# Kernel optimization log

Measured on AMD Instinct MI355X. Metric: run time of the kernel, lower is better.

## Reference

```python
import jax, jax.numpy as jnp
import numpy as np

B = 16       # graphs per batch
N = 256      # nodes per graph (Hi-C submatrix bins)
NT = B * N   # total nodes
E = 131072   # total edges
DIN = 32     # input feature dim (HYPERPARAMETERS['input_shape'])
H1, H2 = 16, 32
HID = 32     # ContactCNN hidden dim
W7 = 7       # final conv width


def setup_inputs() -> dict:
    key = jax.random.key(0)
    ks = jax.random.split(key, 16)
    x = jax.random.normal(ks[0], (NT, DIN), dtype=jnp.float32)
    edge_index = jax.random.randint(ks[1], (2, E), 0, NT, dtype=jnp.int64)
    edge_attr = jax.random.uniform(ks[2], (E,), dtype=jnp.float32)
    batch_index = jnp.repeat(jnp.arange(B, dtype=jnp.int64), N)
    s = 0.1
    params = dict(
        W0=jax.random.normal(ks[3], (DIN, H1), dtype=jnp.float32) * s,
        b0=jnp.zeros((H1,), dtype=jnp.float32),
        W1=jax.random.normal(ks[4], (H1, H2), dtype=jnp.float32) * s,
        b1=jnp.zeros((H2,), dtype=jnp.float32),
        W2=jax.random.normal(ks[5], (H2, H2), dtype=jnp.float32) * s,
        b2=jnp.zeros((H2,), dtype=jnp.float32),
        Wc=jax.random.normal(ks[6], (HID, H2), dtype=jnp.float32) * s,  # 1x1 conv: [out=HID, in=H2]
        bc=jnp.zeros((HID,), dtype=jnp.float32),
        Wp=jax.random.normal(ks[7], (1, HID, W7, W7), dtype=jnp.float32) * s,  # OIHW
        bp=jnp.zeros((1,), dtype=jnp.float32),
    )
    return dict(x=x, edge_index=edge_index, edge_attr=edge_attr,
                batch_index=batch_index, **params)


def _gcn_norm(edge_index, edge_weight, n):
    # PyG gcn_norm with improved=True (self-loop fill value 2.0)
    src, dst = edge_index[0], edge_index[1]
    loop = jnp.arange(n, dtype=src.dtype)
    src_a = jnp.concatenate([src, loop])
    dst_a = jnp.concatenate([dst, loop])
    w_a = jnp.concatenate([edge_weight, jnp.full((n,), 2.0, dtype=edge_weight.dtype)])
    deg = jax.ops.segment_sum(w_a, dst_a, num_segments=n)
    deg_safe = jnp.where(deg > 0, deg, 1.0)
    dinv = jnp.where(deg > 0, jax.lax.rsqrt(deg_safe), 0.0)
    norm = dinv[src_a] * w_a * dinv[dst_a]
    return src_a, dst_a, norm


def _gcn_layer(h, W, b, src_a, dst_a, norm, n):
    h = h @ W                                  # [n, out]
    msg = norm[:, None] * h[src_a]             # gather + scale
    return jax.ops.segment_sum(msg, dst_a, num_segments=n) + b  # scatter-add


def reference(x, edge_index, edge_attr, batch_index,
              W0, b0, W1, b1, W2, b2, Wc, bc, Wp, bp):
    n = x.shape[0]
    src_a, dst_a, norm = _gcn_norm(edge_index, edge_attr, n)
    h = jax.nn.relu(_gcn_layer(x, W0, b0, src_a, dst_a, norm, n))
    h = jax.nn.relu(_gcn_layer(h, W1, b1, src_a, dst_a, norm, n))
    h = jax.nn.relu(_gcn_layer(h, W2, b2, src_a, dst_a, norm, n))
    z = h.reshape(B, N, -1)                    # process_graph_batch
    # ContactCNN: broadcast outer product -> 1x1 conv -> ReLU -> 7x7 conv -> sigmoid
    zm = jnp.einsum('bid,bjd->bdij', z, z)     # [B, D, N, N]
    c = jax.nn.relu(jnp.einsum('bdij,hd->bhij', zm, Wc) + bc[None, :, None, None])
    s = jax.lax.conv_general_dilated(
        c, Wp, window_strides=(1, 1), padding='SAME',
        dimension_numbers=('NCHW', 'OIHW', 'NCHW')) + bp[None, :, None, None]
    return jax.nn.sigmoid(s)                   # [B, 1, N, N]
```

## Files before the change

### kernel.cpp

```cpp
#include <hip/hip_runtime.h>
#include <hip/hip_bf16.h>
#include <hip/hip_fp16.h>

#define NT 4096
#define NE 131072

#define OFF_DEG    0
#define OFF_CNT    16384
#define OFF_FILL   32768
#define OFF_ROWPTR 49152
#define OFF_COL    66048
#define OFF_VAL    590336
#define OFF_G      1114624
#define OFF_HA     1638912
#define OFF_HB     2163200
#define OFF_W2     2687488
#define OFF_C      2695680

typedef __attribute__((ext_vector_type(8))) short bf16x8;
typedef __attribute__((ext_vector_type(4))) float f32x4;
typedef __attribute__((ext_vector_type(2))) __fp16 fp16x2;

__device__ inline unsigned int align16(unsigned int hi, unsigned int lo) {
#if __has_builtin(__builtin_amdgcn_alignbit)
    return __builtin_amdgcn_alignbit(hi, lo, 16);
#else
    return (lo >> 16) | (hi << 16);
#endif
}

__device__ inline unsigned short bfb(float x) {
    return __hip_bfloat16_raw(__float2bfloat16(x)).x;
}


__global__ void k_deg(const int* __restrict__ ei, const float* __restrict__ ew,
                      float* __restrict__ deg, int* __restrict__ cnt) {
    int e = blockIdx.x * 256 + threadIdx.x;
    if (e < NE) {
        int d = ei[NE + e];
        atomicAdd(&deg[d], ew[e]);
        atomicAdd(&cnt[d], 1);
    }
}

__global__ void k_scan(const int* __restrict__ cnt, int* __restrict__ rowptr,
                       float* __restrict__ deg, const float* __restrict__ Wp,
                       unsigned int* __restrict__ w2) {
    __shared__ int sums[1024];
    int t = threadIdx.x;
    #pragma unroll
    for (int k = 0; k < 4; k++) {
        int n = t*4 + k;
        deg[n] = rsqrtf(deg[n] + 2.0f);
    }
    for (int k = t; k < 1568; k += 1024) {
        __half h = __float2half(Wp[k]);
        __half2 hh = __halves2half2(h, h);
        w2[k] = *(unsigned int*)&hh;
    }
    int v0 = cnt[t*4], v1 = cnt[t*4+1], v2 = cnt[t*4+2], v3 = cnt[t*4+3];
    int s = v0 + v1 + v2 + v3;
    sums[t] = s;
    __syncthreads();
    for (int off = 1; off < 1024; off <<= 1) {
        int x = (t >= off) ? sums[t - off] : 0;
        __syncthreads();
        sums[t] += x;
        __syncthreads();
    }
    int excl = sums[t] - s;
    rowptr[t*4]   = excl;
    rowptr[t*4+1] = excl + v0;
    rowptr[t*4+2] = excl + v0 + v1;
    rowptr[t*4+3] = excl + v0 + v1 + v2;
    if (t == 1023) rowptr[NT] = excl + s;
}

__global__ void k_fill(const int* __restrict__ ei, const float* __restrict__ ew,
                       const float* __restrict__ dinv, const int* __restrict__ rowptr,
                       int* __restrict__ fill, int* __restrict__ col, float* __restrict__ val) {
    int e = blockIdx.x * 256 + threadIdx.x;
    if (e < NE) {
        int s = ei[e], d = ei[NE + e];
        int pos = rowptr[d] + atomicAdd(&fill[d], 1);
        col[pos] = s;
        val[pos] = dinv[s] * ew[e] * dinv[d];
    }
}


__global__ void k_mm0(const float* __restrict__ x, const float* __restrict__ W0,
                      float* __restrict__ g) {
    int tid = blockIdx.x * 256 + threadIdx.x;
    int n = tid >> 4, co = tid & 15;
    float acc = 0.f;
    #pragma unroll
    for (int ci = 0; ci < 32; ci++) acc += x[n*32 + ci] * W0[ci*16 + co];
    g[n*16 + co] = acc;
}

__global__ __launch_bounds__(256) void k_agg0(const float* __restrict__ g,
        const float* __restrict__ bias, const float* __restrict__ W1,
        const float* __restrict__ dinv, const int* __restrict__ rowptr,
        const int* __restrict__ col, const float* __restrict__ val,
        float* __restrict__ g1) {
    __shared__ float hs[8][2][16];
    int tid = threadIdx.x;
    int nl = tid >> 5, s = tid & 31, co = s & 15, half = s >> 4;
    int n = blockIdx.x*8 + nl;
    int e0 = rowptr[n], e1 = rowptr[n+1];
    float acc = 0.f;
    if (half == 0) { float dv = dinv[n]; acc = 2.f*dv*dv*g[n*16+co]; }
    int e = e0 + half;
    for (; e + 2 < e1; e += 4) {
        int   c0 = col[e], c1 = col[e+2];
        float v0 = val[e], v1 = val[e+2];
        acc += v0 * g[c0*16+co];
        acc += v1 * g[c1*16+co];
    }
    for (; e < e1; e += 2) acc += val[e] * g[col[e]*16+co];
    hs[nl][half][co] = acc;
    __syncthreads();
    int n2 = tid >> 5, c2 = tid & 31;
    float o = 0.f;
    #pragma unroll
    for (int ci = 0; ci < 16; ci++) {
        float h = fmaxf(hs[n2][0][ci] + hs[n2][1][ci] + bias[ci], 0.f);
        o += h * W1[ci*32 + c2];
    }
    g1[(blockIdx.x*8 + n2)*32 + c2] = o;
}

__global__ __launch_bounds__(256) void k_agg1(const float* __restrict__ g,
        const float* __restrict__ bias, const float* __restrict__ Wn,
        const float* __restrict__ dinv, const int* __restrict__ rowptr,
        const int* __restrict__ col, const float* __restrict__ val,
        float* __restrict__ gn) {
    __shared__ float hs[8][32];
    int tid = threadIdx.x;
    int nl = tid >> 5, co = tid & 31;
    int n = blockIdx.x*8 + nl;
    int e0 = rowptr[n], e1 = rowptr[n+1];
    float dv = dinv[n];
    float acc = 2.f*dv*dv*g[n*32+co];
    int e = e0;
    for (; e + 3 < e1; e += 4) {
        int   c0 = col[e], c1 = col[e+1], c2_ = col[e+2], c3 = col[e+3];
        float v0 = val[e], v1 = val[e+1], v2 = val[e+2], v3 = val[e+3];
        acc += v0 * g[c0*32+co];
        acc += v1 * g[c1*32+co];
        acc += v2 * g[c2_*32+co];
        acc += v3 * g[c3*32+co];
    }
    for (; e < e1; e++) acc += val[e] * g[col[e]*32+co];
    hs[nl][co] = acc;
    __syncthreads();
    float o = 0.f;
    #pragma unroll
    for (int ci = 0; ci < 32; ci++) {
        float h = fmaxf(hs[nl][ci] + bias[ci], 0.f);
        o += h * Wn[ci*32 + co];
    }
    gn[n*32 + co] = o;
}

__global__ __launch_bounds__(256) void k_agg2(const float* __restrict__ g,
        const float* __restrict__ bias,
        const float* __restrict__ dinv, const int* __restrict__ rowptr,
        const int* __restrict__ col, const float* __restrict__ val,
        float* __restrict__ h3) {
    int tid = blockIdx.x*256 + threadIdx.x;
    int n = tid >> 5, co = tid & 31;
    int e0 = rowptr[n], e1 = rowptr[n+1];
    float dv = dinv[n];
    float acc = 2.f*dv*dv*g[n*32+co];
    int e = e0;
    for (; e + 3 < e1; e += 4) {
        int   c0 = col[e], c1 = col[e+1], c2_ = col[e+2], c3 = col[e+3];
        float v0 = val[e], v1 = val[e+1], v2 = val[e+2], v3 = val[e+3];
        acc += v0 * g[c0*32+co];
        acc += v1 * g[c1*32+co];
        acc += v2 * g[c2_*32+co];
        acc += v3 * g[c3*32+co];
    }
    for (; e < e1; e++) acc += val[e] * g[col[e]*32+co];
    h3[n*32 + co] = fmaxf(acc + bias[co], 0.f);
}


__global__ __launch_bounds__(256) void k_c1(const float* __restrict__ z,
                                            const float* __restrict__ Wc,
                                            const float* __restrict__ bc,
                                            unsigned short* __restrict__ c) {
    __shared__ unsigned short zb[256*40];
    __shared__ unsigned short zwb[256*40];
    int blk = blockIdx.x;
    int b = blk >> 5, h = blk & 31;
    int tid = threadIdx.x;
    int lane = tid & 63, w = tid >> 6;
    int m = lane & 15, q = lane >> 4;

    {
        const float4* zp = (const float4*)&z[(b*256 + tid)*32];
        const float4* wp = (const float4*)&Wc[h*32];
        unsigned int ub[16], uw[16];
        #pragma unroll
        for (int r8 = 0; r8 < 8; r8++) {
            float4 f = zp[r8];
            float4 wv = wp[r8];
            ub[r8*2]   = ((unsigned int)bfb(f.y) << 16) | bfb(f.x);
            ub[r8*2+1] = ((unsigned int)bfb(f.w) << 16) | bfb(f.z);
            uw[r8*2]   = ((unsigned int)bfb(f.y*wv.y) << 16) | bfb(f.x*wv.x);
            uw[r8*2+1] = ((unsigned int)bfb(f.w*wv.w) << 16) | bfb(f.z*wv.z);
        }
        uint4* zbp = (uint4*)&zb[tid*40];
        uint4* zwp = (uint4*)&zwb[tid*40];
        #pragma unroll
        for (int k = 0; k < 4; k++) {
            zbp[k] = ((uint4*)ub)[k];
            zwp[k] = ((uint4*)uw)[k];
        }
    }
    __syncthreads();

    bf16x8 bt[16];
    #pragma unroll
    for (int nt = 0; nt < 16; nt++)
        bt[nt] = *(const bf16x8*)&zb[(nt*16 + m)*40 + q*8];

    bf16x8 af[4];
    #pragma unroll
    for (int s = 0; s < 4; s++)
        af[s] = *(const bf16x8*)&zwb[((w*4 + s)*16 + m)*40 + q*8];

    float bch = bc[h];
    size_t plane = ((size_t)blk) << 16;

    #pragma unroll
    for (int s = 0; s < 4; s++) {
        f32x4 acc[16];
        #pragma unroll
        for (int nt = 0; nt < 16; nt++) {
            acc[nt] = (f32x4){0.f, 0.f, 0.f, 0.f};
            acc[nt] = __builtin_amdgcn_mfma_f32_16x16x32_bf16(af[s], bt[nt], acc[nt], 0, 0, 0);
        }
        int jbase = (w*4 + s)*16 + q*4;
        #pragma unroll
        for (int nt = 0; nt < 16; nt++) {
            float v0 = fmaxf(acc[nt][0] + bch, 0.f);
            float v1 = fmaxf(acc[nt][1] + bch, 0.f);
            float v2 = fmaxf(acc[nt][2] + bch, 0.f);
            float v3 = fmaxf(acc[nt][3] + bch, 0.f);
            fp16x2 p0 = __builtin_amdgcn_cvt_pkrtz(v0, v1);
            fp16x2 p1 = __builtin_amdgcn_cvt_pkrtz(v2, v3);
            uint2 o;
            o.x = *(unsigned int*)&p0;
            o.y = *(unsigned int*)&p1;
            *(uint2*)&c[plane + (size_t)(nt*16 + m)*256 + jbase] = o;
        }
    }
}


__global__ __launch_bounds__(256) void k_conv(const __half* __restrict__ c,
                                              const unsigned int* __restrict__ w2,
                                              const float* __restrict__ bp,
                                              float* __restrict__ out) {
    __shared__ __align__(16) unsigned int tile[2][1520];
    int b = blockIdx.z, i0 = blockIdx.y * 32, j0 = blockIdx.x * 64;
    int tid = threadIdx.x;
    int tx = tid & 7, ty = tid >> 3;

    int  goff[6]; int loff[6]; bool gok[6]; bool sok[6];
    #pragma unroll
    for (int k = 0; k < 6; k++) {
        int idx = tid + k*256;
        sok[k] = idx < 1406;
        int r  = idx / 37, cc = idx - r*37;
        int gi = i0 - 3 + r;
        int gdw = (j0 >> 1) - 2 + cc;
        gok[k] = sok[k] && gi >= 0 && gi < 256 && gdw >= 0 && gdw < 128;
        goff[k] = gok[k] ? (gi*128 + gdw) : 0;
        loff[k] = r*40 + cc;
    }

    const unsigned int* cgd = (const unsigned int*)c;

    {
        const unsigned int* cp = cgd + ((size_t)(b*32 + 0) << 15);
        #pragma unroll
        for (int k = 0; k < 6; k++) {
            unsigned int v = gok[k] ? cp[goff[k]] : 0u;
            if (sok[k]) tile[0][loff[k]] = v;
        }
    }
    __syncthreads();

    __half2 acc[4];
    __half2 z2 = __float2half2_rn(0.f);
    acc[0] = z2; acc[1] = z2; acc[2] = z2; acc[3] = z2;

    for (int h = 0; h < 32; h++) {
        unsigned int sv[6];
        if (h < 31) {
            const unsigned int* cp = cgd + ((size_t)(b*32 + h + 1) << 15);
            #pragma unroll
            for (int k = 0; k < 6; k++) sv[k] = gok[k] ? cp[goff[k]] : 0u;
        }

        const unsigned int* T = &tile[h & 1][0];
        const __half2* wrow = (const __half2*)w2 + h*49;
        int rbase = ty*40 + tx*4;
        #pragma unroll
        for (int rl = 0; rl < 7; rl++) {
            const uint4* p = (const uint4*)&T[rbase + rl*40];
            uint4 ua = p[0], ub = p[1];
            unsigned int E[8] = {ua.x, ua.y, ua.z, ua.w, ub.x, ub.y, ub.z, ub.w};
            unsigned int O[7];
            #pragma unroll
            for (int k = 0; k < 7; k++) O[k] = align16(E[k+1], E[k]);
            #pragma unroll
            for (int dj = 0; dj < 7; dj++) {
                __half2 wv = wrow[rl*7 + dj];
                #pragma unroll
                for (int p2 = 0; p2 < 4; p2++) {
                    unsigned int pr = (dj & 1) ? E[p2 + ((dj+1) >> 1)]
                                               : O[p2 + (dj >> 1)];
                    acc[p2] = __hfma2(wv, *(__half2*)&pr, acc[p2]);
                }
            }
        }

        if (h < 31) {
            unsigned int* Tn = &tile[(h+1) & 1][0];
            #pragma unroll
            for (int k = 0; k < 6; k++) if (sok[k]) Tn[loff[k]] = sv[k];
        }
        __syncthreads();
    }

    float bpv = bp[0];
    float res[8];
    #pragma unroll
    for (int p2 = 0; p2 < 4; p2++) {
        float2 f = __half22float2(acc[p2]);
        res[p2*2+0] = 1.0f / (1.0f + __expf(-(f.x + bpv)));
        res[p2*2+1] = 1.0f / (1.0f + __expf(-(f.y + bpv)));
    }
    float4* op = (float4*)&out[((size_t)(b*256 + i0 + ty))*256 + j0 + tx*8];
    op[0] = make_float4(res[0], res[1], res[2], res[3]);
    op[1] = make_float4(res[4], res[5], res[6], res[7]);
}


extern "C" void kernel_launch(void* const* d_in, const int* in_sizes, int n_in,
                              void* d_out, int out_size, void* d_ws, size_t ws_size,
                              hipStream_t stream) {
    const float* x  = (const float*)d_in[0];
    const int*   ei = (const int*)d_in[1];
    const float* ew = (const float*)d_in[2];
    const float* W0 = (const float*)d_in[4];
    const float* b0 = (const float*)d_in[5];
    const float* W1 = (const float*)d_in[6];
    const float* b1 = (const float*)d_in[7];
    const float* W2 = (const float*)d_in[8];
    const float* b2 = (const float*)d_in[9];
    const float* Wc = (const float*)d_in[10];
    const float* bc = (const float*)d_in[11];
    const float* Wp = (const float*)d_in[12];
    const float* bp = (const float*)d_in[13];

    char* ws = (char*)d_ws;
    float* deg    = (float*)(ws + OFF_DEG);
    int*   cnt    = (int*)  (ws + OFF_CNT);
    int*   fill   = (int*)  (ws + OFF_FILL);
    int*   rowptr = (int*)  (ws + OFF_ROWPTR);
    int*   col    = (int*)  (ws + OFF_COL);
    float* val    = (float*)(ws + OFF_VAL);
    float* g0     = (float*)(ws + OFF_G);
    float* g1     = (float*)(ws + OFF_HA);
    float* g2     = (float*)(ws + OFF_HB);
    float* h3     = (float*)(ws + OFF_G);
    unsigned int* w2t = (unsigned int*)(ws + OFF_W2);
    unsigned short* cbuf = (unsigned short*)(ws + OFF_C);

    (void)hipMemsetAsync(d_ws, 0, 49152, stream);

    k_deg <<<NE/256, 256, 0, stream>>>(ei, ew, deg, cnt);
    k_scan<<<1, 1024, 0, stream>>>(cnt, rowptr, deg, Wp, w2t);
    k_fill<<<NE/256, 256, 0, stream>>>(ei, ew, deg, rowptr, fill, col, val);

    k_mm0 <<<NT*16/256, 256, 0, stream>>>(x, W0, g0);
    k_agg0<<<NT/8, 256, 0, stream>>>(g0, b0, W1, deg, rowptr, col, val, g1);
    k_agg1<<<NT/8, 256, 0, stream>>>(g1, b1, W2, deg, rowptr, col, val, g2);
    k_agg2<<<NT*32/256, 256, 0, stream>>>(g2, b2, deg, rowptr, col, val, h3);

    k_c1  <<<512, 256, 0, stream>>>(h3, Wc, bc, cbuf);
    k_conv<<<dim3(4,8,16), 256, 0, stream>>>((const __half*)cbuf, w2t, bp, (float*)d_out);
}
```

Measured before the change: 217.6 us.

## Replace CSR sparse aggregation with dense bf16 adjacency MFMA GEMMs and retile conv

Removes the CSR build (count, scan, fill) and instead scatters normalized edge weights into a dense 4096x4096 bf16 adjacency matrix using packed bf16 atomics. Each GCN layer then becomes a dense MFMA GEMM with the next layer's weight multiply fused in, and node features are kept transposed in bf16. The 7x7 conv is retiled so each thread computes 4 rows by 4 columns, and the intermediate tensors are stored in bf16. This trades gather-heavy sparse work for a 32MB memset plus dense streaming and adds bf16 precision loss, including bf16 accumulation of duplicate edges.

Measured after the change: 237.3 us. 9.1% more time.

```diff
diff --git a/kernel.cpp b/kernel.cpp
--- a/kernel.cpp
+++ b/kernel.cpp
@@ -5,21 +5,17 @@
 #define NT 4096
 #define NE 131072
 
-#define OFF_DEG    0
-#define OFF_CNT    16384
-#define OFF_FILL   32768
-#define OFF_ROWPTR 49152
-#define OFF_COL    66048
-#define OFF_VAL    590336
-#define OFF_G      1114624
-#define OFF_HA     1638912
-#define OFF_HB     2163200
-#define OFF_W2     2687488
-#define OFF_C      2695680
+#define OFF_DEG  0
+#define OFF_A    16384
+#define OFF_G1T  33570816
+#define OFF_G2T  33701888
+#define OFF_G3T  33964032
+#define OFF_C    16384
+#define OFF_H3   67125248
+#define OFF_W2T  67387392
 
 typedef __attribute__((ext_vector_type(8))) short bf16x8;
 typedef __attribute__((ext_vector_type(4))) float f32x4;
-typedef __attribute__((ext_vector_type(2))) __fp16 fp16x2;
 
 __device__ inline unsigned int align16(unsigned int hi, unsigned int lo) {
 #if __has_builtin(__builtin_amdgcn_alignbit)
@@ -33,168 +29,131 @@
     return __hip_bfloat16_raw(__float2bfloat16(x)).x;
 }
 
+__device__ inline void atomic_add_bf16(unsigned short* base, unsigned int idx, float v) {
+    unsigned long long addr = (unsigned long long)(base + (idx & ~1u));
+    unsigned int bits = ((unsigned int)bfb(v)) << ((idx & 1u) * 16);
+    asm volatile("global_atomic_pk_add_bf16 %0, %1, off" :: "v"(addr), "v"(bits) : "memory");
+}
+
 
 __global__ void k_deg(const int* __restrict__ ei, const float* __restrict__ ew,
-                      float* __restrict__ deg, int* __restrict__ cnt) {
+                      float* __restrict__ deg) {
     int e = blockIdx.x * 256 + threadIdx.x;
-    if (e < NE) {
-        int d = ei[NE + e];
-        atomicAdd(&deg[d], ew[e]);
-        atomicAdd(&cnt[d], 1);
-    }
-}
-
-__global__ void k_scan(const int* __restrict__ cnt, int* __restrict__ rowptr,
-                       float* __restrict__ deg, const float* __restrict__ Wp,
-                       unsigned int* __restrict__ w2) {
-    __shared__ int sums[1024];
-    int t = threadIdx.x;
-    #pragma unroll
-    for (int k = 0; k < 4; k++) {
-        int n = t*4 + k;
-        deg[n] = rsqrtf(deg[n] + 2.0f);
-    }
-    for (int k = t; k < 1568; k += 1024) {
-        __half h = __float2half(Wp[k]);
-        __half2 hh = __halves2half2(h, h);
-        w2[k] = *(unsigned int*)&hh;
-    }
-    int v0 = cnt[t*4], v1 = cnt[t*4+1], v2 = cnt[t*4+2], v3 = cnt[t*4+3];
-    int s = v0 + v1 + v2 + v3;
-    sums[t] = s;
-    __syncthreads();
-    for (int off = 1; off < 1024; off <<= 1) {
-        int x = (t >= off) ? sums[t - off] : 0;
-        __syncthreads();
-        sums[t] += x;
-        __syncthreads();
-    }
-    int excl = sums[t] - s;
-    rowptr[t*4]   = excl;
-    rowptr[t*4+1] = excl + v0;
-    rowptr[t*4+2] = excl + v0 + v1;
-    rowptr[t*4+3] = excl + v0 + v1 + v2;
-    if (t == 1023) rowptr[NT] = excl + s;
-}
-
-__global__ void k_fill(const int* __restrict__ ei, const float* __restrict__ ew,
-                       const float* __restrict__ dinv, const int* __restrict__ rowptr,
-                       int* __restrict__ fill, int* __restrict__ col, float* __restrict__ val) {
+    if (e < NE) atomicAdd(&deg[ei[NE + e]], ew[e]);
+}
+
+__global__ void k_scatter(const int* __restrict__ ei, const float* __restrict__ ew,
+                          const float* __restrict__ deg, unsigned short* __restrict__ A16,
+                          const float* __restrict__ x, const float* __restrict__ W0,
+                          unsigned short* __restrict__ G1T,
+                          const float* __restrict__ Wp, unsigned int* __restrict__ w2) {
     int e = blockIdx.x * 256 + threadIdx.x;
     if (e < NE) {
         int s = ei[e], d = ei[NE + e];
-        int pos = rowptr[d] + atomicAdd(&fill[d], 1);
-        col[pos] = s;
-        val[pos] = dinv[s] * ew[e] * dinv[d];
-    }
-}
-
-
-__global__ void k_mm0(const float* __restrict__ x, const float* __restrict__ W0,
-                      float* __restrict__ g) {
-    int tid = blockIdx.x * 256 + threadIdx.x;
-    int n = tid >> 4, co = tid & 15;
-    float acc = 0.f;
-    #pragma unroll
-    for (int ci = 0; ci < 32; ci++) acc += x[n*32 + ci] * W0[ci*16 + co];
-    g[n*16 + co] = acc;
-}
-
-__global__ __launch_bounds__(256) void k_agg0(const float* __restrict__ g,
-        const float* __restrict__ bias, const float* __restrict__ W1,
-        const float* __restrict__ dinv, const int* __restrict__ rowptr,
-        const int* __restrict__ col, const float* __restrict__ val,
-        float* __restrict__ g1) {
-    __shared__ float hs[8][2][16];
+        float v = rsqrtf(deg[s] + 2.f) * ew[e] * rsqrtf(deg[d] + 2.f);
+        atomic_add_bf16(A16, (unsigned int)d * 4096u + (unsigned int)s, v);
+    }
+    if (e < NT) {
+        atomic_add_bf16(A16, (unsigned int)e * 4097u, 2.f / (deg[e] + 2.f));
+    }
+    if (e < NT * 16) {
+        int node = e & 4095, co = e >> 12;
+        const float4* xr = (const float4*)(x + node * 32);
+        float a = 0.f;
+        #pragma unroll
+        for (int r = 0; r < 8; r++) {
+            float4 f = xr[r];
+            a += f.x * W0[(r*4+0)*16 + co] + f.y * W0[(r*4+1)*16 + co]
+               + f.z * W0[(r*4+2)*16 + co] + f.w * W0[(r*4+3)*16 + co];
+        }
+        G1T[co * 4096 + node] = bfb(a);
+    }
+    if (e >= NE - 1568) {
+        int k = e - (NE - 1568);
+        __half hh = __float2half(Wp[k]);
+        __half2 h2 = __halves2half2(hh, hh);
+        w2[k] = *(unsigned int*)&h2;
+    }
+}
+
+
+template <int NIN, int NOUT, bool LAST>
+__global__ __launch_bounds__(512) void k_gcn(const unsigned short* __restrict__ A16,
+                                             const unsigned short* __restrict__ Gt,
+                                             const float* __restrict__ bias,
+                                             const float* __restrict__ W,
+                                             unsigned short* __restrict__ Gout) {
+    constexpr int T = NIN / 16;
+    __shared__ float red[8][T][16][16];
+    __shared__ unsigned short wtile[16 * 40];
+    int mt = blockIdx.x;
     int tid = threadIdx.x;
-    int nl = tid >> 5, s = tid & 31, co = s & 15, half = s >> 4;
-    int n = blockIdx.x*8 + nl;
-    int e0 = rowptr[n], e1 = rowptr[n+1];
-    float acc = 0.f;
-    if (half == 0) { float dv = dinv[n]; acc = 2.f*dv*dv*g[n*16+co]; }
-    int e = e0 + half;
-    for (; e + 2 < e1; e += 4) {
-        int   c0 = col[e], c1 = col[e+2];
-        float v0 = val[e], v1 = val[e+2];
-        acc += v0 * g[c0*16+co];
-        acc += v1 * g[c1*16+co];
-    }
-    for (; e < e1; e += 2) acc += val[e] * g[col[e]*16+co];
-    hs[nl][half][co] = acc;
+    int w = tid >> 6, lane = tid & 63, m = lane & 15, q = lane >> 4;
+    int kw = w * 512;
+
+    const unsigned short* arow = A16 + (size_t)(mt * 16 + m) * 4096 + kw + q * 8;
+    f32x4 acc[T];
+    #pragma unroll
+    for (int t = 0; t < T; t++) acc[t] = (f32x4){0.f, 0.f, 0.f, 0.f};
+
+    bf16x8 wfrag;
+    if (!LAST && w < NOUT / 16) {
+        #pragma unroll
+        for (int j = 0; j < 8; j++) {
+            int ci = q * 8 + j;
+            wfrag[j] = (ci < NIN) ? (short)bfb(W[ci * NOUT + w * 16 + m]) : (short)0;
+        }
+    }
+
+    #pragma unroll 4
+    for (int s = 0; s < 16; s++) {
+        bf16x8 bA = *(const bf16x8*)(arow + s * 32);
+        #pragma unroll
+        for (int t = 0; t < T; t++) {
+            bf16x8 af = *(const bf16x8*)(Gt + (size_t)(t * 16 + m) * 4096 + kw + q * 8 + s * 32);
+            acc[t] = __builtin_amdgcn_mfma_f32_16x16x32_bf16(af, bA, acc[t], 0, 0, 0);
+        }
+    }
+    #pragma unroll
+    for (int t = 0; t < T; t++)
+        #pragma unroll
+        for (int r = 0; r < 4; r++) red[w][t][q*4 + r][m] = acc[t][r];
     __syncthreads();
-    int n2 = tid >> 5, c2 = tid & 31;
-    float o = 0.f;
-    #pragma unroll
-    for (int ci = 0; ci < 16; ci++) {
-        float h = fmaxf(hs[n2][0][ci] + hs[n2][1][ci] + bias[ci], 0.f);
-        o += h * W1[ci*32 + c2];
-    }
-    g1[(blockIdx.x*8 + n2)*32 + c2] = o;
-}
-
-__global__ __launch_bounds__(256) void k_agg1(const float* __restrict__ g,
-        const float* __restrict__ bias, const float* __restrict__ Wn,
-        const float* __restrict__ dinv, const int* __restrict__ rowptr,
-        const int* __restrict__ col, const float* __restrict__ val,
-        float* __restrict__ gn) {
-    __shared__ float hs[8][32];
-    int tid = threadIdx.x;
-    int nl = tid >> 5, co = tid & 31;
-    int n = blockIdx.x*8 + nl;
-    int e0 = rowptr[n], e1 = rowptr[n+1];
-    float dv = dinv[n];
-    float acc = 2.f*dv*dv*g[n*32+co];
-    int e = e0;
-    for (; e + 3 < e1; e += 4) {
-        int   c0 = col[e], c1 = col[e+1], c2_ = col[e+2], c3 = col[e+3];
-        float v0 = val[e], v1 = val[e+1], v2 = val[e+2], v3 = val[e+3];
-        acc += v0 * g[c0*32+co];
-        acc += v1 * g[c1*32+co];
-        acc += v2 * g[c2_*32+co];
-        acc += v3 * g[c3*32+co];
-    }
-    for (; e < e1; e++) acc += val[e] * g[col[e]*32+co];
-    hs[nl][co] = acc;
+
+    if (tid < T * 256) {
+        int dstp = tid & 15, cop = (tid >> 4) & 15, t = tid >> 8;
+        float sum = 0.f;
+        #pragma unroll
+        for (int w8 = 0; w8 < 8; w8++) sum += red[w8][t][cop][dstp];
+        int co = t * 16 + cop;
+        float val = fmaxf(sum + bias[co], 0.f);
+        if (LAST) Gout[(size_t)(mt * 16 + dstp) * 32 + co] = bfb(val);
+        else      wtile[dstp * 40 + co] = bfb(val);
+    }
+    if (!LAST && NIN == 16 && tid >= 256 && tid < 512) {
+        int idx = tid - 256;
+        wtile[(idx & 15) * 40 + 16 + ((idx >> 4) & 15)] = 0;
+    }
     __syncthreads();
-    float o = 0.f;
-    #pragma unroll
-    for (int ci = 0; ci < 32; ci++) {
-        float h = fmaxf(hs[nl][ci] + bias[ci], 0.f);
-        o += h * Wn[ci*32 + co];
-    }
-    gn[n*32 + co] = o;
-}
-
-__global__ __launch_bounds__(256) void k_agg2(const float* __restrict__ g,
-        const float* __restrict__ bias,
-        const float* __restrict__ dinv, const int* __restrict__ rowptr,
-        const int* __restrict__ col, const float* __restrict__ val,
-        float* __restrict__ h3) {
-    int tid = blockIdx.x*256 + threadIdx.x;
-    int n = tid >> 5, co = tid & 31;
-    int e0 = rowptr[n], e1 = rowptr[n+1];
-    float dv = dinv[n];
-    float acc = 2.f*dv*dv*g[n*32+co];
-    int e = e0;
-    for (; e + 3 < e1; e += 4) {
-        int   c0 = col[e], c1 = col[e+1], c2_ = col[e+2], c3 = col[e+3];
-        float v0 = val[e], v1 = val[e+1], v2 = val[e+2], v3 = val[e+3];
-        acc += v0 * g[c0*32+co];
-        acc += v1 * g[c1*32+co];
-        acc += v2 * g[c2_*32+co];
-        acc += v3 * g[c3*32+co];
-    }
-    for (; e < e1; e++) acc += val[e] * g[col[e]*32+co];
-    h3[n*32 + co] = fmaxf(acc + bias[co], 0.f);
-}
-
-
-__global__ __launch_bounds__(256) void k_c1(const float* __restrict__ z,
+
+    if (!LAST && w < NOUT / 16) {
+        bf16x8 af = *(const bf16x8*)&wtile[m * 40 + q * 8];
+        f32x4 o = (f32x4){0.f, 0.f, 0.f, 0.f};
+        o = __builtin_amdgcn_mfma_f32_16x16x32_bf16(af, wfrag, o, 0, 0, 0);
+        uint2 ov;
+        ov.x = (unsigned int)bfb(o[0]) | ((unsigned int)bfb(o[1]) << 16);
+        ov.y = (unsigned int)bfb(o[2]) | ((unsigned int)bfb(o[3]) << 16);
+        *(uint2*)&Gout[(size_t)(w * 16 + m) * 4096 + mt * 16 + q * 4] = ov;
+    }
+}
+
+
+__global__ __launch_bounds__(256) void k_c1(const unsigned short* __restrict__ h3,
                                             const float* __restrict__ Wc,
                                             const float* __restrict__ bc,
                                             unsigned short* __restrict__ c) {
-    __shared__ unsigned short zb[256*40];
-    __shared__ unsigned short zwb[256*40];
+    __shared__ unsigned short zb[256 * 40];
+    __shared__ unsigned short zwb[256 * 40];
     int blk = blockIdx.x;
     int b = blk >> 5, h = blk & 31;
     int tid = threadIdx.x;
@@ -202,23 +161,24 @@
     int m = lane & 15, q = lane >> 4;
 
     {
-        const float4* zp = (const float4*)&z[(b*256 + tid)*32];
-        const float4* wp = (const float4*)&Wc[h*32];
-        unsigned int ub[16], uw[16];
-        #pragma unroll
-        for (int r8 = 0; r8 < 8; r8++) {
-            float4 f = zp[r8];
-            float4 wv = wp[r8];
-            ub[r8*2]   = ((unsigned int)bfb(f.y) << 16) | bfb(f.x);
-            ub[r8*2+1] = ((unsigned int)bfb(f.w) << 16) | bfb(f.z);
-            uw[r8*2]   = ((unsigned int)bfb(f.y*wv.y) << 16) | bfb(f.x*wv.x);
-            uw[r8*2+1] = ((unsigned int)bfb(f.w*wv.w) << 16) | bfb(f.z*wv.z);
-        }
-        uint4* zbp = (uint4*)&zb[tid*40];
-        uint4* zwp = (uint4*)&zwb[tid*40];
+        const uint4* zp = (const uint4*)(h3 + (size_t)(b * 256 + tid) * 32);
+        unsigned int zr[16];
+        #pragma unroll
+        for (int k = 0; k < 4; k++) ((uint4*)zr)[k] = zp[k];
+        unsigned int uw[16];
+        #pragma unroll
+        for (int k = 0; k < 16; k++) {
+            float lo = __uint_as_float(zr[k] << 16);
+            float hi = __uint_as_float(zr[k] & 0xffff0000u);
+            float wl = Wc[h * 32 + 2 * k];
+            float wh = Wc[h * 32 + 2 * k + 1];
+            uw[k] = (unsigned int)bfb(lo * wl) | ((unsigned int)bfb(hi * wh) << 16);
+        }
+        uint4* zbp = (uint4*)&zb[tid * 40];
+        uint4* zwp = (uint4*)&zwb[tid * 40];
         #pragma unroll
         for (int k = 0; k < 4; k++) {
-            zbp[k] = ((uint4*)ub)[k];
+            zbp[k] = ((uint4*)zr)[k];
             zwp[k] = ((uint4*)uw)[k];
         }
     }
@@ -227,12 +187,12 @@
     bf16x8 bt[16];
     #pragma unroll
     for (int nt = 0; nt < 16; nt++)
-        bt[nt] = *(const bf16x8*)&zb[(nt*16 + m)*40 + q*8];
+        bt[nt] = *(const bf16x8*)&zb[(nt * 16 + m) * 40 + q * 8];
 
     bf16x8 af[4];
     #pragma unroll
     for (int s = 0; s < 4; s++)
-        af[s] = *(const bf16x8*)&zwb[((w*4 + s)*16 + m)*40 + q*8];
+        af[s] = *(const bf16x8*)&zwb[((w * 4 + s) * 16 + m) * 40 + q * 8];
 
     float bch = bc[h];
     size_t plane = ((size_t)blk) << 16;
@@ -245,19 +205,19 @@
             acc[nt] = (f32x4){0.f, 0.f, 0.f, 0.f};
             acc[nt] = __builtin_amdgcn_mfma_f32_16x16x32_bf16(af[s], bt[nt], acc[nt], 0, 0, 0);
         }
-        int jbase = (w*4 + s)*16 + q*4;
+        int jbase = (w * 4 + s) * 16 + q * 4;
         #pragma unroll
         for (int nt = 0; nt < 16; nt++) {
             float v0 = fmaxf(acc[nt][0] + bch, 0.f);
             float v1 = fmaxf(acc[nt][1] + bch, 0.f);
             float v2 = fmaxf(acc[nt][2] + bch, 0.f);
             float v3 = fmaxf(acc[nt][3] + bch, 0.f);
-            fp16x2 p0 = __builtin_amdgcn_cvt_pkrtz(v0, v1);
-            fp16x2 p1 = __builtin_amdgcn_cvt_pkrtz(v2, v3);
+            __half2 p0 = __floats2half2_rn(v0, v1);
+            __half2 p1 = __floats2half2_rn(v2, v3);
             uint2 o;
             o.x = *(unsigned int*)&p0;
             o.y = *(unsigned int*)&p1;
-            *(uint2*)&c[plane + (size_t)(nt*16 + m)*256 + jbase] = o;
+            *(uint2*)&c[plane + (size_t)(nt * 16 + m) * 256 + jbase] = o;
         }
     }
 }
@@ -267,90 +227,96 @@
                                               const unsigned int* __restrict__ w2,
                                               const float* __restrict__ bp,
                                               float* __restrict__ out) {
-    __shared__ __align__(16) unsigned int tile[2][1520];
-    int b = blockIdx.z, i0 = blockIdx.y * 32, j0 = blockIdx.x * 64;
+    __shared__ __align__(16) unsigned int tile[2][70 * 38];
+    int b = blockIdx.z, i0 = blockIdx.y * 64, j0 = blockIdx.x * 64;
     int tid = threadIdx.x;
-    int tx = tid & 7, ty = tid >> 3;
-
-    int  goff[6]; int loff[6]; bool gok[6]; bool sok[6];
-    #pragma unroll
-    for (int k = 0; k < 6; k++) {
-        int idx = tid + k*256;
-        sok[k] = idx < 1406;
-        int r  = idx / 37, cc = idx - r*37;
+    int tx = tid & 15, ty = tid >> 4;
+
+    int goff[11]; int loff[11]; bool gok[11]; bool sok[11];
+    #pragma unroll
+    for (int k = 0; k < 11; k++) {
+        int idx = tid + k * 256;
+        sok[k] = idx < 2590;
+        int r = idx / 37, cc = idx - r * 37;
         int gi = i0 - 3 + r;
         int gdw = (j0 >> 1) - 2 + cc;
         gok[k] = sok[k] && gi >= 0 && gi < 256 && gdw >= 0 && gdw < 128;
-        goff[k] = gok[k] ? (gi*128 + gdw) : 0;
-        loff[k] = r*40 + cc;
+        goff[k] = gok[k] ? (gi * 128 + gdw) : 0;
+        loff[k] = r * 38 + cc;
     }
 
     const unsigned int* cgd = (const unsigned int*)c;
-
     {
-        const unsigned int* cp = cgd + ((size_t)(b*32 + 0) << 15);
-        #pragma unroll
-        for (int k = 0; k < 6; k++) {
+        const unsigned int* cp = cgd + ((size_t)(b * 32) << 15);
+        #pragma unroll
+        for (int k = 0; k < 11; k++) {
             unsigned int v = gok[k] ? cp[goff[k]] : 0u;
             if (sok[k]) tile[0][loff[k]] = v;
         }
     }
     __syncthreads();
 
-    __half2 acc[4];
+    __half2 acc[4][2];
     __half2 z2 = __float2half2_rn(0.f);
-    acc[0] = z2; acc[1] = z2; acc[2] = z2; acc[3] = z2;
+    #pragma unroll
+    for (int o = 0; o < 4; o++) { acc[o][0] = z2; acc[o][1] = z2; }
 
     for (int h = 0; h < 32; h++) {
-        unsigned int sv[6];
+        unsigned int sv[11];
         if (h < 31) {
-            const unsigned int* cp = cgd + ((size_t)(b*32 + h + 1) << 15);
+            const unsigned int* cp = cgd + ((size_t)(b * 32 + h + 1) << 15);
             #pragma unroll
-            for (int k = 0; k < 6; k++) sv[k] = gok[k] ? cp[goff[k]] : 0u;
+            for (int k = 0; k < 11; k++) sv[k] = gok[k] ? cp[goff[k]] : 0u;
         }
 
         const unsigned int* T = &tile[h & 1][0];
-        const __half2* wrow = (const __half2*)w2 + h*49;
-        int rbase = ty*40 + tx*4;
-        #pragma unroll
-        for (int rl = 0; rl < 7; rl++) {
-            const uint4* p = (const uint4*)&T[rbase + rl*40];
-            uint4 ua = p[0], ub = p[1];
-            unsigned int E[8] = {ua.x, ua.y, ua.z, ua.w, ub.x, ub.y, ub.z, ub.w};
-            unsigned int O[7];
+        const __half2* wrow = (const __half2*)w2 + h * 49;
+        #pragma unroll
+        for (int r8 = 0; r8 < 10; r8++) {
+            const unsigned int* rp = T + (ty * 4 + r8) * 38 + tx * 2;
+            uint2 ea = *(const uint2*)rp;
+            uint2 eb = *(const uint2*)(rp + 2);
+            uint2 ec = *(const uint2*)(rp + 4);
+            unsigned int E[6] = {ea.x, ea.y, eb.x, eb.y, ec.x, ec.y};
+            unsigned int O[5];
             #pragma unroll
-            for (int k = 0; k < 7; k++) O[k] = align16(E[k+1], E[k]);
+            for (int k = 0; k < 5; k++) O[k] = align16(E[k + 1], E[k]);
             #pragma unroll
-            for (int dj = 0; dj < 7; dj++) {
-                __half2 wv = wrow[rl*7 + dj];
+            for (int o = 0; o < 4; o++) {
+                int di = r8 - o;
+                if (di < 0 || di > 6) continue;
                 #pragma unroll
-                for (int p2 = 0; p2 < 4; p2++) {
-                    unsigned int pr = (dj & 1) ? E[p2 + ((dj+1) >> 1)]
-                                               : O[p2 + (dj >> 1)];
-                    acc[p2] = __hfma2(wv, *(__half2*)&pr, acc[p2]);
+                for (int dj = 0; dj < 7; dj++) {
+                    __half2 wv = wrow[di * 7 + dj];
+                    int d = dj - 3;
+                    unsigned int p0 = (d & 1) ? O[(d + 3) >> 1] : E[(d + 4) >> 1];
+                    unsigned int p1 = (d & 1) ? O[((d + 3) >> 1) + 1] : E[((d + 4) >> 1) + 1];
+                    acc[o][0] = __hfma2(wv, *(__half2*)&p0, acc[o][0]);
+                    acc[o][1] = __hfma2(wv, *(__half2*)&p1, acc[o][1]);
                 }
             }
         }
 
         if (h < 31) {
-            unsigned int* Tn = &tile[(h+1) & 1][0];
+            unsigned int* Tn = &tile[(h + 1) & 1][0];
             #pragma unroll
-            for (int k = 0; k < 6; k++) if (sok[k]) Tn[loff[k]] = sv[k];
+            for (int k = 0; k < 11; k++) if (sok[k]) Tn[loff[k]] = sv[k];
         }
         __syncthreads();
     }
 
     float bpv = bp[0];
-    float res[8];
-    #pragma unroll
-    for (int p2 = 0; p2 < 4; p2++) {
-        float2 f = __half22float2(acc[p2]);
-        res[p2*2+0] = 1.0f / (1.0f + __expf(-(f.x + bpv)));
-        res[p2*2+1] = 1.0f / (1.0f + __expf(-(f.y + bpv)));
-    }
-    float4* op = (float4*)&out[((size_t)(b*256 + i0 + ty))*256 + j0 + tx*8];
-    op[0] = make_float4(res[0], res[1], res[2], res[3]);
-    op[1] = make_float4(res[4], res[5], res[6], res[7]);
+    #pragma unroll
+    for (int o = 0; o < 4; o++) {
+        float2 f0 = __half22float2(acc[o][0]);
+        float2 f1 = __half22float2(acc[o][1]);
+        float4 r;
+        r.x = 1.0f / (1.0f + __expf(-(f0.x + bpv)));
+        r.y = 1.0f / (1.0f + __expf(-(f0.y + bpv)));
+        r.z = 1.0f / (1.0f + __expf(-(f1.x + bpv)));
+        r.w = 1.0f / (1.0f + __expf(-(f1.y + bpv)));
+        *(float4*)&out[((size_t)(b * 256 + i0 + ty * 4 + o)) * 256 + j0 + tx * 4] = r;
+    }
 }
 
 
@@ -372,30 +338,24 @@
     const float* bp = (const float*)d_in[13];
 
     char* ws = (char*)d_ws;
-    float* deg    = (float*)(ws + OFF_DEG);
-    int*   cnt    = (int*)  (ws + OFF_CNT);
-    int*   fill   = (int*)  (ws + OFF_FILL);
-    int*   rowptr = (int*)  (ws + OFF_ROWPTR);
-    int*   col    = (int*)  (ws + OFF_COL);
-    float* val    = (float*)(ws + OFF_VAL);
-    float* g0     = (float*)(ws + OFF_G);
-    float* g1     = (float*)(ws + OFF_HA);
-    float* g2     = (float*)(ws + OFF_HB);
-    float* h3     = (float*)(ws + OFF_G);
-    unsigned int* w2t = (unsigned int*)(ws + OFF_W2);
+    float*          deg  = (float*)(ws + OFF_DEG);
+    unsigned short* A16  = (unsigned short*)(ws + OFF_A);
+    unsigned short* G1T  = (unsigned short*)(ws + OFF_G1T);
+    unsigned short* G2T  = (unsigned short*)(ws + OFF_G2T);
+    unsigned short* G3T  = (unsigned short*)(ws + OFF_G3T);
+    unsigned short* H3   = (unsigned short*)(ws + OFF_H3);
+    unsigned int*   w2t  = (unsigned int*)(ws + OFF_W2T);
     unsigned short* cbuf = (unsigned short*)(ws + OFF_C);
 
-    (void)hipMemsetAsync(d_ws, 0, 49152, stream);
-
-    k_deg <<<NE/256, 256, 0, stream>>>(ei, ew, deg, cnt);
-    k_scan<<<1, 1024, 0, stream>>>(cnt, rowptr, deg, Wp, w2t);
-    k_fill<<<NE/256, 256, 0, stream>>>(ei, ew, deg, rowptr, fill, col, val);
-
-    k_mm0 <<<NT*16/256, 256, 0, stream>>>(x, W0, g0);
-    k_agg0<<<NT/8, 256, 0, stream>>>(g0, b0, W1, deg, rowptr, col, val, g1);
-    k_agg1<<<NT/8, 256, 0, stream>>>(g1, b1, W2, deg, rowptr, col, val, g2);
-    k_agg2<<<NT*32/256, 256, 0, stream>>>(g2, b2, deg, rowptr, col, val, h3);
-
-    k_c1  <<<512, 256, 0, stream>>>(h3, Wc, bc, cbuf);
-    k_conv<<<dim3(4,8,16), 256, 0, stream>>>((const __half*)cbuf, w2t, bp, (float*)d_out);
-}
+    (void)hipMemsetAsync(d_ws, 0, 16384 + 33554432, stream);
+
+    k_deg    <<<NE/256, 256, 0, stream>>>(ei, ew, deg);
+    k_scatter<<<NE/256, 256, 0, stream>>>(ei, ew, deg, A16, x, W0, G1T, Wp, w2t);
+
+    k_gcn<16, 32, false><<<256, 512, 0, stream>>>(A16, G1T, b0, W1, G2T);
+    k_gcn<32, 32, false><<<256, 512, 0, stream>>>(A16, G2T, b1, W2, G3T);
+    k_gcn<32, 32, true> <<<256, 512, 0, stream>>>(A16, G3T, b2, nullptr, H3);
+
+    k_c1  <<<512, 256, 0, stream>>>(H3, Wc, bc, cbuf);
+    k_conv<<<dim3(4,4,16), 256, 0, stream>>>((const __half*)cbuf, w2t, bp, (float*)d_out);
+}
```
